# Optimization experiments

Measured on AMD Instinct MI355X. Metric: run time of the kernel, lower is better.

Reference implementation:

```python
import jax, jax.numpy as jnp
import numpy as np

NUC_DIM = 256
ELE_DIM = 256
HID_DIM = 256
NUM_HEADS = 4
HEAD_DIM = HID_DIM // NUM_HEADS


def setup_inputs() -> dict:
    key = jax.random.key(0)
    ks = jax.random.split(key, 10)
    B, N, M = 8, 2048, 4096
    s_nuc = 1.0 / np.sqrt(NUC_DIM)
    s_ele = 1.0 / np.sqrt(ELE_DIM)
    s_hid = 1.0 / np.sqrt(HID_DIM)
    return {
        "nuclear_features": jax.random.normal(ks[0], (B, N, NUC_DIM), jnp.float32),
        "electronic_features": jax.random.normal(ks[1], (B, M, ELE_DIM), jnp.float32),
        "Wq": jax.random.uniform(ks[2], (NUC_DIM, HID_DIM), jnp.float32, -s_nuc, s_nuc),
        "bq": jax.random.uniform(ks[3], (HID_DIM,), jnp.float32, -s_nuc, s_nuc),
        "Wk": jax.random.uniform(ks[4], (ELE_DIM, HID_DIM), jnp.float32, -s_ele, s_ele),
        "bk": jax.random.uniform(ks[5], (HID_DIM,), jnp.float32, -s_ele, s_ele),
        "Wv": jax.random.uniform(ks[6], (ELE_DIM, HID_DIM), jnp.float32, -s_ele, s_ele),
        "bv": jax.random.uniform(ks[7], (HID_DIM,), jnp.float32, -s_ele, s_ele),
        "Wo": jax.random.uniform(ks[8], (HID_DIM, NUC_DIM), jnp.float32, -s_hid, s_hid),
        "bo": jax.random.uniform(ks[9], (NUC_DIM,), jnp.float32, -s_hid, s_hid),
    }


def reference(nuclear_features, electronic_features, Wq, bq, Wk, bk, Wv, bv, Wo, bo):
    B, N, _ = nuclear_features.shape
    _, M, _ = electronic_features.shape
    H, D = NUM_HEADS, HEAD_DIM
    q = (nuclear_features @ Wq + bq).reshape(B, N, H, D)
    k = (electronic_features @ Wk + bk).reshape(B, M, H, D)
    v = (electronic_features @ Wv + bv).reshape(B, M, H, D)
    # scores: [B, N, M, H] (matches torch einsum layout)
    scores = jnp.einsum('bnhd,bmhd->bnmh', q, k) / jnp.sqrt(jnp.float32(D))
    attn = jax.nn.softmax(scores, axis=2)  # softmax over M
    out = jnp.einsum('bnmh,bmhd->bnhd', attn, v).reshape(B, N, H * D)
    return out @ Wo + bo
```

## Files before the change

### kernel.cpp

```cpp
#include <hip/hip_runtime.h>

typedef __bf16 bf16;
typedef bf16 bf16x8 __attribute__((ext_vector_type(8)));
typedef bf16 bf16x4 __attribute__((ext_vector_type(4)));
typedef float f32x4 __attribute__((ext_vector_type(4)));
typedef float f32x8 __attribute__((ext_vector_type(8)));
typedef float f32x16 __attribute__((ext_vector_type(16)));
typedef unsigned int u32;

#define BB 8
#define NN 2048
#define MM 4096

#if defined(__has_builtin)
#if __has_builtin(__builtin_amdgcn_exp2f)
#define EXP2(x) __builtin_amdgcn_exp2f(x)
#endif
#endif
#ifndef EXP2
#define EXP2(x) exp2f(x)
#endif

__global__ __launch_bounds__(256) void prep_wt(
    const float* W0, const float* W1, const float* W2, const float* W3,
    bf16* T0, bf16* T1, bf16* T2, bf16* T3) {
  const float* W; bf16* T;
  switch (blockIdx.y) {
    case 0:  W = W0; T = T0; break;
    case 1:  W = W1; T = T1; break;
    case 2:  W = W2; T = T2; break;
    default: W = W3; T = T3; break;
  }
  int n = blockIdx.x, k = threadIdx.x;
  T[n * 256 + k] = (bf16)W[k * 256 + n];
}

template<int AM, int CM>
__global__ __launch_bounds__(256) void gemm_bias(
    const void* Aptr, const bf16* Wt, const float* bias, const float* bias2,
    void* Cout, float scale) {
  __shared__ __align__(16) char smem[32768];
  bf16* As = (bf16*)smem;
  bf16* Bs = (bf16*)(smem + 16384);
  const int t = threadIdx.x;
  const int lane = t & 63, wid = t >> 6;
  const int l15 = lane & 15, lhi = lane >> 4, l7 = lane & 7;
  const int row0 = blockIdx.x * 128, col0 = blockIdx.y * 128;
  const int wm = (wid >> 1) * 64, wn = (wid & 1) * 64;

  f32x4 zero4 = {0.f, 0.f, 0.f, 0.f};
  f32x4 acc[4][4];
#pragma unroll
  for (int i = 0; i < 4; ++i)
#pragma unroll
    for (int j = 0; j < 4; ++j) acc[i][j] = zero4;

  for (int k0 = 0; k0 < 256; k0 += 64) {
    __syncthreads();
    if (AM == 0) {
      const float* Af = (const float*)Aptr;
#pragma unroll
      for (int i = 0; i < 8; ++i) {
        int idx = t + i * 256;
        int m = idx >> 4, c4 = idx & 15;
        f32x4 v = *(const f32x4*)(Af + (size_t)(row0 + m) * 256 + k0 + c4 * 4);
        bf16x4 bv;
#pragma unroll
        for (int j = 0; j < 4; ++j) bv[j] = (bf16)v[j];
        *(bf16x4*)((char*)As + m * 128 + ((c4 * 8) ^ ((m & 7) << 4))) = bv;
      }
    } else {
      const bf16* Ab = (const bf16*)Aptr;
#pragma unroll
      for (int i = 0; i < 4; ++i) {
        int idx = t + i * 256;
        int m = idx >> 3, c = idx & 7;
        int r = row0 + m;
        int b = r >> 11, nl = r & 2047, h = k0 >> 6;
        const bf16* src = Ab + ((size_t)(b * 4 + h) * 2048 + nl) * 64 + c * 8;
        bf16x8 v = *(const bf16x8*)src;
        *(bf16x8*)((char*)As + m * 128 + ((c * 16) ^ ((m & 7) << 4))) = v;
      }
    }
#pragma unroll
    for (int i = 0; i < 4; ++i) {
      int idx = t + i * 256;
      int n = idx >> 3, c = idx & 7;
      bf16x8 v = *(const bf16x8*)(Wt + (size_t)(col0 + n) * 256 + k0 + c * 8);
      *(bf16x8*)((char*)Bs + n * 128 + ((c * 16) ^ ((n & 7) << 4))) = v;
    }
    __syncthreads();
#pragma unroll
    for (int kh = 0; kh < 2; ++kh) {
      bf16x8 a[4], b[4];
#pragma unroll
      for (int mi = 0; mi < 4; ++mi) {
        int row = wm + mi * 16 + l15;
        a[mi] = *(const bf16x8*)((char*)As + row * 128 + ((kh * 64 + lhi * 16) ^ (l7 << 4)));
      }
#pragma unroll
      for (int ni = 0; ni < 4; ++ni) {
        int row = wn + ni * 16 + l15;
        b[ni] = *(const bf16x8*)((char*)Bs + row * 128 + ((kh * 64 + lhi * 16) ^ (l7 << 4)));
      }
#pragma unroll
      for (int mi = 0; mi < 4; ++mi)
#pragma unroll
        for (int ni = 0; ni < 4; ++ni)
          acc[mi][ni] = __builtin_amdgcn_mfma_f32_16x16x32_bf16(a[mi], b[ni], acc[mi][ni], 0, 0, 0);
    }
  }

  if (CM == 4) __syncthreads();

#pragma unroll
  for (int mi = 0; mi < 4; ++mi)
#pragma unroll
    for (int ni = 0; ni < 4; ++ni) {
      int n = col0 + wn + ni * 16 + l15;
      float bvv = (CM == 4) ? (n < 256 ? bias[n] : bias2[n - 256]) : bias[n];
#pragma unroll
      for (int r = 0; r < 4; ++r) {
        int mrow = row0 + wm + mi * 16 + lhi * 4 + r;
        float val = (acc[mi][ni][r] + bvv) * scale;
        if (CM == 0) {
          ((float*)Cout)[(size_t)mrow * 256 + n] = val;
        } else if (CM == 1) {
          int b = mrow >> 11, nl = mrow & 2047;
          ((bf16*)Cout)[((size_t)(b * 4 + (n >> 6)) * 2048 + nl) * 64 + (n & 63)] = (bf16)val;
        } else {
          int dm = wm + mi * 16 + lhi * 4 + r;
          int dn = wn + ni * 16 + l15;
          int dkt = dm >> 6, kvl = dm & 63;
          int dh = dn >> 6, d = dn & 63;
          int inner;
          if (col0 < 256)
            inner = (((kvl >> 5) & 1) << 12) + ((d >> 3) << 9)
                  + ((kvl & 31) << 4) + ((d & 7) << 1);
          else
            inner = ((d >> 5) << 12) + (((kvl >> 3) & 7) << 9)
                  + ((d & 31) << 4) + ((kvl & 7) << 1);
          *(bf16*)(smem + (dkt * 2 + dh) * 8192 + inner) = (bf16)val;
        }
      }
    }

  if (CM == 4) {
    __syncthreads();
    const int isK = (col0 < 256);
    int b = row0 >> 12, kt0 = (row0 & 4095) >> 6, h0 = (col0 & 255) >> 6;
#pragma unroll
    for (int c = 0; c < 4; ++c) {
      int dkt = c >> 1, dh = c & 1;
      char* dst = (char*)Cout + ((size_t)((b * 4 + h0 + dh) * 64 + kt0 + dkt)) * 16384
                  + (isK ? 0 : 8192);
      *(bf16x8*)(dst + t * 16)        = *(const bf16x8*)(smem + c * 8192 + t * 16);
      *(bf16x8*)(dst + 4096 + t * 16) = *(const bf16x8*)(smem + c * 8192 + 4096 + t * 16);
    }
  }
}

__device__ __forceinline__ u32 pkbf(float a, float b) {
  union { bf16 h[2]; u32 u; } p;
  p.h[0] = (bf16)a; p.h[1] = (bf16)b;
  return p.u;
}

__global__ __launch_bounds__(512) void attn_kernel(
    const bf16* __restrict__ q, const char* __restrict__ kvt,
    bf16* __restrict__ ao) {
  __shared__ __align__(16) char lds[2][2][16384];
  __shared__ float Ll[8][32];
  const int t = threadIdx.x;
  const int lane = t & 63, wid = t >> 6;
  const int l31 = lane & 31, lhi1 = lane >> 5;
  const int bid = blockIdx.x;
  const int xcd = bid & 7, rem = bid >> 3;
  const int bh = (xcd << 2) + (rem >> 4);
  const int q0 = (rem & 15) * 128;
  const int qt = wid >> 1, kvh = wid & 1;

  bf16x8 qf[4];
  {
    const bf16* qp = q + ((size_t)bh * NN + q0 + qt * 32 + l31) * 64 + lhi1 * 8;
#pragma unroll
    for (int c = 0; c < 4; ++c) qf[c] = *(const bf16x8*)(qp + c * 16);
  }

  const char* sp = kvt + ((size_t)(bh * 64 + kvh * 32)) * 16384 + qt * 4096 + lane * 16;
  char* wp0 = &lds[kvh][0][qt * 4096 + lane * 16];
  char* wp1 = &lds[kvh][1][qt * 4096 + lane * 16];
  const char* KB0 = &lds[kvh][0][0];
  const char* KB1 = &lds[kvh][1][0];

  f32x16 O0 = {}, O1 = {}, psum = {};

  bf16x8 st0, st1, st2, st3;
#define SLOAD()                                                           \
  {                                                                       \
    st0 = *(const bf16x8*)(sp);                                           \
    st1 = *(const bf16x8*)(sp + 1024);                                    \
    st2 = *(const bf16x8*)(sp + 2048);                                    \
    st3 = *(const bf16x8*)(sp + 3072);                                    \
    sp += 16384;                                                          \
  }
#define SWRITE(WP)                                                        \
  {                                                                       \
    *(bf16x8*)(WP) = st0;                                                 \
    *(bf16x8*)((WP) + 1024) = st1;                                        \
    *(bf16x8*)((WP) + 2048) = st2;                                        \
    *(bf16x8*)((WP) + 3072) = st3;                                        \
  }

  auto compute = [&](const char* KB) {
    const char* VB = KB + 8192;
    f32x16 s0 = {}, s1 = {};
    __builtin_amdgcn_s_setprio(1);
#pragma unroll
    for (int kc = 0; kc < 4; ++kc) {
      bf16x8 k0 = *(const bf16x8*)(KB + ((2 * kc + lhi1) << 9) + l31 * 16);
      bf16x8 k1 = *(const bf16x8*)(KB + 4096 + ((2 * kc + lhi1) << 9) + l31 * 16);
      s0 = __builtin_amdgcn_mfma_f32_32x32x16_bf16(k0, qf[kc], s0, 0, 0, 0);
      s1 = __builtin_amdgcn_mfma_f32_32x32x16_bf16(k1, qf[kc], s1, 0, 0, 0);
    }
    __builtin_amdgcn_s_setprio(0);

#pragma unroll
    for (int r = 0; r < 16; ++r) {
      s0[r] = EXP2(s0[r]);
      s1[r] = EXP2(s1[r]);
    }
    psum += s0 + s1;

    u32 w0[8], w1[8];
#pragma unroll
    for (int s = 0; s < 4; ++s)
#pragma unroll
      for (int rr = 0; rr < 2; ++rr) {
        w0[s * 2 + rr] = pkbf(s0[4 * s + 2 * rr], s0[4 * s + 2 * rr + 1]);
        w1[s * 2 + rr] = pkbf(s1[4 * s + 2 * rr], s1[4 * s + 2 * rr + 1]);
      }

    __builtin_amdgcn_s_setprio(1);
#pragma unroll
    for (int t2 = 0; t2 < 2; ++t2) {
#pragma unroll
      for (int c2 = 0; c2 < 2; ++c2) {
        u32 aw0 = t2 ? w1[4 * c2 + 0] : w0[4 * c2 + 0];
        u32 aw1 = t2 ? w1[4 * c2 + 1] : w0[4 * c2 + 1];
        u32 bw0 = t2 ? w1[4 * c2 + 2] : w0[4 * c2 + 2];
        u32 bw1 = t2 ? w1[4 * c2 + 3] : w0[4 * c2 + 3];
        asm("v_permlane32_swap_b32 %0, %1" : "+v"(aw0), "+v"(bw0));
        asm("v_permlane32_swap_b32 %0, %1" : "+v"(aw1), "+v"(bw1));
        union { u32 u[4]; bf16x8 v; } pb;
        pb.u[0] = aw0;
        pb.u[1] = aw1;
        pb.u[2] = bw0;
        pb.u[3] = bw1;
        const int kb = t2 * 2 + c2;
        int base = ((2 * kb + lhi1) << 9) + l31 * 16;
        bf16x8 va = *(const bf16x8*)(VB + base);
        bf16x8 vb = *(const bf16x8*)(VB + 4096 + base);
        O0 = __builtin_amdgcn_mfma_f32_32x32x16_bf16(va, pb.v, O0, 0, 0, 0);
        O1 = __builtin_amdgcn_mfma_f32_32x32x16_bf16(vb, pb.v, O1, 0, 0, 0);
      }
    }
    __builtin_amdgcn_s_setprio(0);
  };

  SLOAD(); SWRITE(wp0);
  __syncthreads();

  for (int kt = 0; kt < 32; kt += 2) {
    SLOAD();
    compute(KB0);
    SWRITE(wp1);
    __syncthreads();
    if (kt + 2 < 32) SLOAD();
    compute(KB1);
    if (kt + 2 < 32) SWRITE(wp0);
    __syncthreads();
  }

  f32x8 v8 = __builtin_shufflevector(psum, psum, 0, 1, 2, 3, 4, 5, 6, 7) +
             __builtin_shufflevector(psum, psum, 8, 9, 10, 11, 12, 13, 14, 15);
  f32x4 v4 = __builtin_shufflevector(v8, v8, 0, 1, 2, 3) +
             __builtin_shufflevector(v8, v8, 4, 5, 6, 7);
  float ss = (v4[0] + v4[1]) + (v4[2] + v4[3]);
  float l = ss + __shfl_xor(ss, 32);

  float* Olf = (float*)&lds[0][0][0];
#pragma unroll
  for (int t2 = 0; t2 < 2; ++t2)
#pragma unroll
    for (int r = 0; r < 16; ++r) {
      int d = t2 * 32 + (r & 3) + 8 * (r >> 2) + 4 * lhi1;
      Olf[wid * 2048 + d * 32 + l31] = t2 ? O1[r] : O0[r];
    }
  if (lane < 32) Ll[wid][l31] = l;
  __syncthreads();

  const int pw = wid ^ 1;
  float inv = 1.f / (l + Ll[pw][l31]);
  const int dth = kvh;
  f32x16 Os = dth ? O1 : O0;
  bf16* op = ao + ((size_t)bh * NN + q0 + qt * 32 + l31) * 64 + dth * 32 + 4 * lhi1;
#pragma unroll
  for (int rg = 0; rg < 4; ++rg) {
    bf16x4 ov;
#pragma unroll
    for (int e = 0; e < 4; ++e) {
      int r = rg * 4 + e;
      int d = dth * 32 + e + 8 * rg + 4 * lhi1;
      float comb = Os[r] + Olf[pw * 2048 + d * 32 + l31];
      ov[e] = (bf16)(comb * inv);
    }
    *(bf16x4*)(op + 8 * rg) = ov;
  }
#undef SLOAD
#undef SWRITE
}

extern "C" void kernel_launch(void* const* d_in, const int* in_sizes, int n_in,
                              void* d_out, int out_size, void* d_ws, size_t ws_size,
                              hipStream_t stream) {
  const float* nuc = (const float*)d_in[0];
  const float* ele = (const float*)d_in[1];
  const float* Wq  = (const float*)d_in[2];
  const float* bq  = (const float*)d_in[3];
  const float* Wk  = (const float*)d_in[4];
  const float* bk  = (const float*)d_in[5];
  const float* Wv  = (const float*)d_in[6];
  const float* bv  = (const float*)d_in[7];
  const float* Wo  = (const float*)d_in[8];
  const float* bo  = (const float*)d_in[9];
  float* out = (float*)d_out;
  char* ws = (char*)d_ws;

  bf16* wtq  = (bf16*)(ws + 0);
  bf16* wtkv = (bf16*)(ws + 131072);
  bf16* wtk  = (bf16*)(ws + 131072);
  bf16* wtv  = (bf16*)(ws + 262144);
  bf16* wto  = (bf16*)(ws + 393216);
  bf16* qhs  = (bf16*)(ws + 524288);
  char* kvt  = (char*)(ws + 8912896);
  bf16* aoh  = (bf16*)(ws + 42467328);

  prep_wt<<<dim3(256, 4), 256, 0, stream>>>(Wq, Wk, Wv, Wo, wtq, wtk, wtv, wto);

  gemm_bias<0, 1><<<dim3(128, 2), 256, 0, stream>>>(nuc, wtq, bq, nullptr, qhs, 0.18033688011112042f);
  gemm_bias<0, 4><<<dim3(256, 4), 256, 0, stream>>>(ele, wtkv, bk, bv, kvt, 1.0f);

  attn_kernel<<<dim3(512), 512, 0, stream>>>(qhs, kvt, aoh);

  gemm_bias<1, 0><<<dim3(128, 2), 256, 0, stream>>>(aoh, wto, bo, nullptr, out, 1.0f);
}
```

Baseline: 139.6 us.

## Drop KV split across wave pairs in attention kernel, use 256-thread blocks

Each wave now processes its 32 queries over the full KV sequence (64 tiles) instead of two waves splitting KV halves and merging partial outputs through shared memory. This removes the LDS combine step, the extra barrier and the partial-sum exchange, and halves LDS use per block. The cost is half as many waves per block, so there is less parallelism per CU and a longer serial loop per wave, which may reduce latency hiding.

After: 150.0 us. 1.07x slower.

```diff
diff --git a/kernel.cpp b/kernel.cpp
--- a/kernel.cpp
+++ b/kernel.cpp
@@ -166,11 +166,10 @@
   return p.u;
 }
 
-__global__ __launch_bounds__(512) void attn_kernel(
+__global__ __launch_bounds__(256) void attn_kernel(
     const bf16* __restrict__ q, const char* __restrict__ kvt,
     bf16* __restrict__ ao) {
-  __shared__ __align__(16) char lds[2][2][16384];
-  __shared__ float Ll[8][32];
+  __shared__ __align__(16) char lds[2][16384];
   const int t = threadIdx.x;
   const int lane = t & 63, wid = t >> 6;
   const int l31 = lane & 31, lhi1 = lane >> 5;
@@ -178,20 +177,19 @@
   const int xcd = bid & 7, rem = bid >> 3;
   const int bh = (xcd << 2) + (rem >> 4);
   const int q0 = (rem & 15) * 128;
-  const int qt = wid >> 1, kvh = wid & 1;
 
   bf16x8 qf[4];
   {
-    const bf16* qp = q + ((size_t)bh * NN + q0 + qt * 32 + l31) * 64 + lhi1 * 8;
+    const bf16* qp = q + ((size_t)bh * NN + q0 + wid * 32 + l31) * 64 + lhi1 * 8;
 #pragma unroll
     for (int c = 0; c < 4; ++c) qf[c] = *(const bf16x8*)(qp + c * 16);
   }
 
-  const char* sp = kvt + ((size_t)(bh * 64 + kvh * 32)) * 16384 + qt * 4096 + lane * 16;
-  char* wp0 = &lds[kvh][0][qt * 4096 + lane * 16];
-  char* wp1 = &lds[kvh][1][qt * 4096 + lane * 16];
-  const char* KB0 = &lds[kvh][0][0];
-  const char* KB1 = &lds[kvh][1][0];
+  const char* sp = kvt + ((size_t)bh * 64) * 16384 + t * 16;
+  char* wp0 = &lds[0][t * 16];
+  char* wp1 = &lds[1][t * 16];
+  const char* KB0 = &lds[0][0];
+  const char* KB1 = &lds[1][0];
 
   f32x16 O0 = {}, O1 = {}, psum = {};
 
@@ -199,17 +197,17 @@
 #define SLOAD()                                                           \
   {                                                                       \
     st0 = *(const bf16x8*)(sp);                                           \
-    st1 = *(const bf16x8*)(sp + 1024);                                    \
-    st2 = *(const bf16x8*)(sp + 2048);                                    \
-    st3 = *(const bf16x8*)(sp + 3072);                                    \
+    st1 = *(const bf16x8*)(sp + 4096);                                    \
+    st2 = *(const bf16x8*)(sp + 8192);                                    \
+    st3 = *(const bf16x8*)(sp + 12288);                                   \
     sp += 16384;                                                          \
   }
-#define SWRITE(WP)                                                        \
+#define SWRITE(WP)                                                       \
   {                                                                       \
     *(bf16x8*)(WP) = st0;                                                 \
-    *(bf16x8*)((WP) + 1024) = st1;                                        \
-    *(bf16x8*)((WP) + 2048) = st2;                                        \
-    *(bf16x8*)((WP) + 3072) = st3;                                        \
+    *(bf16x8*)((WP) + 4096) = st1;                                        \
+    *(bf16x8*)((WP) + 8192) = st2;                                        \
+    *(bf16x8*)((WP) + 12288) = st3;                                       \
   }
 
   auto compute = [&](const char* KB) {
@@ -271,14 +269,14 @@
   SLOAD(); SWRITE(wp0);
   __syncthreads();
 
-  for (int kt = 0; kt < 32; kt += 2) {
+  for (int kt = 0; kt < 64; kt += 2) {
     SLOAD();
     compute(KB0);
     SWRITE(wp1);
     __syncthreads();
-    if (kt + 2 < 32) SLOAD();
+    if (kt + 2 < 64) SLOAD();
     compute(KB1);
-    if (kt + 2 < 32) SWRITE(wp0);
+    if (kt + 2 < 64) SWRITE(wp0);
     __syncthreads();
   }
 
@@ -289,33 +287,18 @@
   float ss = (v4[0] + v4[1]) + (v4[2] + v4[3]);
   float l = ss + __shfl_xor(ss, 32);
 
-  float* Olf = (float*)&lds[0][0][0];
-#pragma unroll
-  for (int t2 = 0; t2 < 2; ++t2)
-#pragma unroll
-    for (int r = 0; r < 16; ++r) {
-      int d = t2 * 32 + (r & 3) + 8 * (r >> 2) + 4 * lhi1;
-      Olf[wid * 2048 + d * 32 + l31] = t2 ? O1[r] : O0[r];
-    }
-  if (lane < 32) Ll[wid][l31] = l;
-  __syncthreads();
-
-  const int pw = wid ^ 1;
-  float inv = 1.f / (l + Ll[pw][l31]);
-  const int dth = kvh;
-  f32x16 Os = dth ? O1 : O0;
-  bf16* op = ao + ((size_t)bh * NN + q0 + qt * 32 + l31) * 64 + dth * 32 + 4 * lhi1;
+  float inv = 1.f / l;
+  bf16* op = ao + ((size_t)bh * NN + q0 + wid * 32 + l31) * 64 + 4 * lhi1;
 #pragma unroll
   for (int rg = 0; rg < 4; ++rg) {
-    bf16x4 ov;
+    bf16x4 o0, o1;
 #pragma unroll
     for (int e = 0; e < 4; ++e) {
-      int r = rg * 4 + e;
-      int d = dth * 32 + e + 8 * rg + 4 * lhi1;
-      float comb = Os[r] + Olf[pw * 2048 + d * 32 + l31];
-      ov[e] = (bf16)(comb * inv);
-    }
-    *(bf16x4*)(op + 8 * rg) = ov;
+      o0[e] = (bf16)(O0[rg * 4 + e] * inv);
+      o1[e] = (bf16)(O1[rg * 4 + e] * inv);
+    }
+    *(bf16x4*)(op + 8 * rg) = o0;
+    *(bf16x4*)(op + 32 + 8 * rg) = o1;
   }
 #undef SLOAD
 #undef SWRITE
@@ -351,7 +334,7 @@
   gemm_bias<0, 1><<<dim3(128, 2), 256, 0, stream>>>(nuc, wtq, bq, nullptr, qhs, 0.18033688011112042f);
   gemm_bias<0, 4><<<dim3(256, 4), 256, 0, stream>>>(ele, wtkv, bk, bv, kvt, 1.0f);
 
-  attn_kernel<<<dim3(512), 512, 0, stream>>>(qhs, kvt, aoh);
+  attn_kernel<<<dim3(512), 256, 0, stream>>>(qhs, kvt, aoh);
 
   gemm_bias<1, 0><<<dim3(128, 2), 256, 0, stream>>>(aoh, wto, bo, nullptr, out, 1.0f);
 }
```

## Deepen K/V global prefetch to two tiles ahead and drop setprio hints

Applied to the files above, without the earlier changes.

The attention loop now holds two register staging sets (A and B) for K/V tiles, so global loads are issued two tiles ahead of their use instead of one. LDS writes move to the start of each half-iteration, giving global loads a full compute phase to land and putting more time between each load and its LDS store. The s_setprio hints around the MFMA blocks are also removed. The cost is sixteen more VGPRs for staging, which could reduce occupancy, and changed wave scheduling without the priority hints.

New measurement: 140.9 us. About the same (+0.9%).

```diff
diff --git a/kernel.cpp b/kernel.cpp
--- a/kernel.cpp
+++ b/kernel.cpp
@@ -195,27 +195,41 @@
 
   f32x16 O0 = {}, O1 = {}, psum = {};
 
-  bf16x8 st0, st1, st2, st3;
-#define SLOAD()                                                           \
+  bf16x8 sA0, sA1, sA2, sA3, sB0, sB1, sB2, sB3;
+#define SLOADA()                                                          \
   {                                                                       \
-    st0 = *(const bf16x8*)(sp);                                           \
-    st1 = *(const bf16x8*)(sp + 1024);                                    \
-    st2 = *(const bf16x8*)(sp + 2048);                                    \
-    st3 = *(const bf16x8*)(sp + 3072);                                    \
+    sA0 = *(const bf16x8*)(sp);                                           \
+    sA1 = *(const bf16x8*)(sp + 1024);                                    \
+    sA2 = *(const bf16x8*)(sp + 2048);                                    \
+    sA3 = *(const bf16x8*)(sp + 3072);                                    \
     sp += 16384;                                                          \
   }
-#define SWRITE(WP)                                                        \
+#define SLOADB()                                                          \
   {                                                                       \
-    *(bf16x8*)(WP) = st0;                                                 \
-    *(bf16x8*)((WP) + 1024) = st1;                                        \
-    *(bf16x8*)((WP) + 2048) = st2;                                        \
-    *(bf16x8*)((WP) + 3072) = st3;                                        \
+    sB0 = *(const bf16x8*)(sp);                                           \
+    sB1 = *(const bf16x8*)(sp + 1024);                                    \
+    sB2 = *(const bf16x8*)(sp + 2048);                                    \
+    sB3 = *(const bf16x8*)(sp + 3072);                                    \
+    sp += 16384;                                                          \
+  }
+#define SWRITEA(WP)                                                       \
+  {                                                                       \
+    *(bf16x8*)(WP) = sA0;                                                 \
+    *(bf16x8*)((WP) + 1024) = sA1;                                        \
+    *(bf16x8*)((WP) + 2048) = sA2;                                        \
+    *(bf16x8*)((WP) + 3072) = sA3;                                        \
+  }
+#define SWRITEB(WP)                                                       \
+  {                                                                       \
+    *(bf16x8*)(WP) = sB0;                                                 \
+    *(bf16x8*)((WP) + 1024) = sB1;                                        \
+    *(bf16x8*)((WP) + 2048) = sB2;                                        \
+    *(bf16x8*)((WP) + 3072) = sB3;                                        \
   }
 
   auto compute = [&](const char* KB) {
     const char* VB = KB + 8192;
     f32x16 s0 = {}, s1 = {};
-    __builtin_amdgcn_s_setprio(1);
 #pragma unroll
     for (int kc = 0; kc < 4; ++kc) {
       bf16x8 k0 = *(const bf16x8*)(KB + ((2 * kc + lhi1) << 9) + l31 * 16);
@@ -223,7 +237,6 @@
       s0 = __builtin_amdgcn_mfma_f32_32x32x16_bf16(k0, qf[kc], s0, 0, 0, 0);
       s1 = __builtin_amdgcn_mfma_f32_32x32x16_bf16(k1, qf[kc], s1, 0, 0, 0);
     }
-    __builtin_amdgcn_s_setprio(0);
 
 #pragma unroll
     for (int r = 0; r < 16; ++r) {
@@ -241,7 +254,6 @@
         w1[s * 2 + rr] = pkbf(s1[4 * s + 2 * rr], s1[4 * s + 2 * rr + 1]);
       }
 
-    __builtin_amdgcn_s_setprio(1);
 #pragma unroll
     for (int t2 = 0; t2 < 2; ++t2) {
 #pragma unroll
@@ -265,20 +277,23 @@
         O1 = __builtin_amdgcn_mfma_f32_32x32x16_bf16(vb, pb.v, O1, 0, 0, 0);
       }
     }
-    __builtin_amdgcn_s_setprio(0);
   };
 
-  SLOAD(); SWRITE(wp0);
+  SLOADA(); SWRITEA(wp0);
+  SLOADA();
+  SLOADB();
   __syncthreads();
 
   for (int kt = 0; kt < 32; kt += 2) {
-    SLOAD();
+    SWRITEA(wp1);
+    if (kt + 3 < 32) SLOADA();
     compute(KB0);
-    SWRITE(wp1);
-    __syncthreads();
-    if (kt + 2 < 32) SLOAD();
+    __syncthreads();
+    if (kt + 2 < 32) {
+      SWRITEB(wp0);
+      if (kt + 4 < 32) SLOADB();
+    }
     compute(KB1);
-    if (kt + 2 < 32) SWRITE(wp0);
     __syncthreads();
   }
 
@@ -317,8 +332,10 @@
     }
     *(bf16x4*)(op + 8 * rg) = ov;
   }
-#undef SLOAD
-#undef SWRITE
+#undef SLOADA
+#undef SLOADB
+#undef SWRITEA
+#undef SWRITEB
 }
 
 extern "C" void kernel_launch(void* const* d_in, const int* in_sizes, int n_in,
```
